# Optimization experiments

Hardware: AMD Instinct MI355X
Metric: run time of the kernel (lower is better)

Reference implementation:

```python
import jax, jax.numpy as jnp
import numpy as np

TEMPERATURE = 0.1
WINDOW = 7  # torch loop: k in range(1, min(8, seq_len - i)) -> offsets 1..7


def _normalize(x, axis=-1, eps=1e-12):
    # F.normalize: x / max(||x||, eps)
    n = jnp.linalg.norm(x, axis=axis, keepdims=True)
    return x / jnp.maximum(n, eps)


def setup_inputs() -> dict:
    key = jax.random.key(0)
    k1, k2 = jax.random.split(key, 2)
    states = jax.random.normal(k1, (4, 16, 1024, 256), dtype=jnp.float32)
    patterns = jax.random.normal(k2, (64, 256), dtype=jnp.float32)
    transfer_weights = jnp.zeros((16, 64, 64), dtype=jnp.float32)
    return {"states": states, "patterns": patterns, "transfer_weights": transfer_weights}


def _forward(states, patterns, transfer_weights):
    b, h, s, d = states.shape
    # --- detect_patterns: similarity to normalized pattern library + softmax ---
    sims = jnp.einsum('bhsd,pd->bhsp', states, _normalize(patterns))
    pattern_scores = jax.nn.softmax(sims / TEMPERATURE, axis=-1)  # [b,h,s,p]

    # --- compute_routing_scores: grad of states.sum() wrt states is ones ->
    #     grad_norm = ||ones||_2 over dim = sqrt(d) (constant), softmax over seq ---
    grad_norm = jnp.full((b, h, s), jnp.sqrt(jnp.float32(d)), dtype=states.dtype)
    routing_scores = jax.nn.softmax(grad_norm / TEMPERATURE, axis=-1)  # uniform [b,h,s]

    # --- optimize_routing: windowed min-plus shortest-path DP ---
    # torch keeps distances [b,h,s,s] but every slice along dim 2 is identical
    # (init and updates only index the last axis), so carry a [b,h,s] vector
    # and broadcast at the end. Pad by WINDOW so near-end updates land in pad.
    inf = jnp.float32(np.inf)
    dist0 = jnp.full((b, h, s + WINDOW), inf, dtype=states.dtype).at[..., 0].set(0.0)
    cost_pad = jnp.pad(-routing_scores, ((0, 0), (0, 0), (0, WINDOW)))

    def step(dist, i):
        cur = jax.lax.dynamic_slice_in_dim(dist, i, 1, axis=-1)          # [b,h,1]
        win = jax.lax.dynamic_slice_in_dim(dist, i + 1, WINDOW, axis=-1)  # [b,h,W]
        c = jax.lax.dynamic_slice_in_dim(cost_pad, i + 1, WINDOW, axis=-1)
        new = jnp.minimum(win, cur + c)
        dist = jax.lax.dynamic_update_slice_in_dim(dist, new, i + 1, axis=-1)
        return dist, None

    dist, _ = jax.lax.scan(step, dist0, jnp.arange(s - 1))
    d_final = dist[..., :s]                                  # [b,h,s]
    optimal_routes = jnp.broadcast_to(d_final[:, :, None, :], (b, h, s, s))

    return routing_scores, optimal_routes, transfer_weights, pattern_scores


def reference(states, patterns, transfer_weights):
    return _forward(states, patterns, transfer_weights)
```

## Files before the change

### kernel.cpp

```cpp
#include <hip/hip_runtime.h>
#include <math.h>

constexpr int B = 4, H = 16, S = 1024, D = 256, P = 64;
constexpr long long N_ROWS = (long long)B * H * S;
constexpr long long OFF_RT = 0;
constexpr long long SZ_RT  = N_ROWS;
constexpr long long OFF_OR = OFF_RT + SZ_RT;
constexpr long long SZ_OR  = N_ROWS * (long long)S;
constexpr long long OFF_TW = OFF_OR + SZ_OR;
constexpr long long SZ_TW  = 16LL * 64 * 64;
constexpr long long OFF_PS = OFF_TW + SZ_TW;

typedef _Float16 half8   __attribute__((ext_vector_type(8)));
typedef _Float16 half4v  __attribute__((ext_vector_type(4)));
typedef float    floatx4 __attribute__((ext_vector_type(4)));

constexpr int BSTRIDE = 264;

__global__ __launch_bounds__(64) void k_normalize(const float* __restrict__ pat,
                                                  _Float16* __restrict__ pnh,
                                                  _Float16* __restrict__ pnl) {
    int p    = blockIdx.x;
    int lane = threadIdx.x;
    const floatx4* src = (const floatx4*)(pat + (long long)p * D);
    floatx4 v = src[lane];
    float ss = v.x * v.x + v.y * v.y + v.z * v.z + v.w * v.w;
    #pragma unroll
    for (int m = 1; m < 64; m <<= 1) ss += __shfl_xor(ss, m, 64);
    float scale = 10.0f / fmaxf(sqrtf(ss), 1e-12f);
    float a[4] = { v.x * scale, v.y * scale, v.z * scale, v.w * scale };
    half4v hh, ll;
    #pragma unroll
    for (int j = 0; j < 4; ++j) {
        _Float16 h = (_Float16)a[j];
        hh[j] = h;
        ll[j] = (_Float16)(a[j] - (float)h);
    }
    *(half4v*)(pnh + (long long)p * D + lane * 4) = hh;
    *(half4v*)(pnl + (long long)p * D + lane * 4) = ll;
}

__global__ __launch_bounds__(256) void k_routes_small(
        floatx4* __restrict__ routes,
        const floatx4* __restrict__ tw,
        float* __restrict__ out) {
    long long blk = blockIdx.x;
    int t = threadIdx.x;
    if (blk < 65536) {
        long long i = blk * 256 + t;
        int j0 = (int)((i << 2) & (S - 1));
        float b0 = (float)j0 * (-0.0009765625f);
        floatx4 v;
        v.x = b0;
        v.y = b0 - 0.0009765625f;
        v.z = b0 - 0.001953125f;
        v.w = b0 - 0.0029296875f;
        routes[i] = v;
    } else {
        int i = (int)(blk - 65536) * 256 + t;
        constexpr int Q = (int)SZ_RT / 4;
        if (i < Q) {
            floatx4 v = { 0.0009765625f, 0.0009765625f,
                          0.0009765625f, 0.0009765625f };
            ((floatx4*)(out + OFF_RT))[i] = v;
        } else {
            ((floatx4*)(out + OFF_TW))[i - Q] = tw[i - Q];
        }
    }
}

__global__ __launch_bounds__(256) void k_gemm_mfma(
        const float* __restrict__ states,
        const _Float16* __restrict__ pnh,
        const _Float16* __restrict__ pnl,
        float* __restrict__ out_ps) {
    __shared__ _Float16 smem[2 * P * BSTRIDE];
    _Float16* smH = smem;
    _Float16* smL = smem + P * BSTRIDE;

    int tid  = threadIdx.x;
    {
        const half8* gh = (const half8*)pnh;
        const half8* gl = (const half8*)pnl;
        #pragma unroll
        for (int it = 0; it < 8; ++it) {
            int idx = it * 256 + tid;
            int row = idx >> 5;
            int c8  = idx & 31;
            *(half8*)&smH[row * BSTRIDE + c8 * 8] = gh[idx];
            *(half8*)&smL[row * BSTRIDE + c8 * 8] = gl[idx];
        }
    }
    __syncthreads();

    int wave = tid >> 6;
    int lane = tid & 63;
    int q    = lane >> 4;
    int m    = lane & 15;
    long long row0 = (long long)blockIdx.x * 64 + wave * 16;
    const float* __restrict__ arow = states + (row0 + m) * D + q * 8;

    floatx4 acc[4] = {floatx4{0,0,0,0}, floatx4{0,0,0,0},
                      floatx4{0,0,0,0}, floatx4{0,0,0,0}};

    float4 n0 = *(const float4*)(arow);
    float4 n1 = *(const float4*)(arow + 4);
    #pragma unroll
    for (int kk = 0; kk < 8; ++kk) {
        float4 a0 = n0, a1 = n1;
        if (kk < 7) {
            n0 = *(const float4*)(arow + (kk + 1) * 32);
            n1 = *(const float4*)(arow + (kk + 1) * 32 + 4);
        }
        float av[8] = { a0.x, a0.y, a0.z, a0.w, a1.x, a1.y, a1.z, a1.w };
        half8 ah, al;
        #pragma unroll
        for (int j = 0; j < 8; ++j) {
            _Float16 h = (_Float16)av[j];
            ah[j] = h;
            al[j] = (_Float16)(av[j] - (float)h);
        }
        #pragma unroll
        for (int t = 0; t < 4; ++t) {
            int boff = (t * 16 + m) * BSTRIDE + kk * 32 + q * 8;
            half8 bh = *(const half8*)&smH[boff];
            half8 bl = *(const half8*)&smL[boff];
            acc[t] = __builtin_amdgcn_mfma_f32_16x16x32_f16(ah, bh, acc[t], 0, 0, 0);
            acc[t] = __builtin_amdgcn_mfma_f32_16x16x32_f16(al, bh, acc[t], 0, 0, 0);
            acc[t] = __builtin_amdgcn_mfma_f32_16x16x32_f16(ah, bl, acc[t], 0, 0, 0);
        }
    }

    float e[4][4];
    #pragma unroll
    for (int r = 0; r < 4; ++r) {
        float mx = fmaxf(fmaxf(acc[0][r], acc[1][r]), fmaxf(acc[2][r], acc[3][r]));
        #pragma unroll
        for (int msk = 1; msk < 16; msk <<= 1) mx = fmaxf(mx, __shfl_xor(mx, msk, 64));
        float s = 0.0f;
        #pragma unroll
        for (int t = 0; t < 4; ++t) { e[t][r] = __expf(acc[t][r] - mx); s += e[t][r]; }
        #pragma unroll
        for (int msk = 1; msk < 16; msk <<= 1) s += __shfl_xor(s, msk, 64);
        float inv = 1.0f / s;
        long long row = row0 + q * 4 + r;
        #pragma unroll
        for (int t = 0; t < 4; ++t) {
            out_ps[row * P + t * 16 + m] = e[t][r] * inv;
        }
    }
}

extern "C" void kernel_launch(void* const* d_in, const int* in_sizes, int n_in,
                              void* d_out, int out_size, void* d_ws, size_t ws_size,
                              hipStream_t stream) {
    const float* states   = (const float*)d_in[0];
    const float* patterns = (const float*)d_in[1];
    const float* transfer = (const float*)d_in[2];
    float* out = (float*)d_out;
    _Float16* pnh = (_Float16*)d_ws;
    _Float16* pnl = pnh + P * D;

    k_normalize<<<dim3(P), dim3(64), 0, stream>>>(patterns, pnh, pnl);

    k_routes_small<<<dim3(65536 + 128), dim3(256), 0, stream>>>(
        (floatx4*)(out + OFF_OR), (const floatx4*)transfer, out);

    k_gemm_mfma<<<dim3(1024), dim3(256), 0, stream>>>(states, pnh, pnl, out + OFF_PS);
}
```

Baseline: 330.9 us.

## Fold pattern normalization into fill kernel and double rows per wave in GEMM

The separate pattern-normalize kernel is merged into the routes/fill kernel as 16 extra blocks, which removes one kernel launch. The GEMM kernel now has each wave process 32 rows instead of 16 with two accumulator sets, and the grid is halved to 512 blocks. This reuses each LDS B-fragment load across twice as many MFMAs and gives the loads more independent work to hide behind. The cost is higher register pressure and fewer blocks to spread across the CUs.

```diff
diff --git a/kernel.cpp b/kernel.cpp
--- a/kernel.cpp
+++ b/kernel.cpp
@@ -17,33 +17,13 @@
 
 constexpr int BSTRIDE = 264;
 
-__global__ __launch_bounds__(64) void k_normalize(const float* __restrict__ pat,
-                                                  _Float16* __restrict__ pnh,
-                                                  _Float16* __restrict__ pnl) {
-    int p    = blockIdx.x;
-    int lane = threadIdx.x;
-    const floatx4* src = (const floatx4*)(pat + (long long)p * D);
-    floatx4 v = src[lane];
-    float ss = v.x * v.x + v.y * v.y + v.z * v.z + v.w * v.w;
-    #pragma unroll
-    for (int m = 1; m < 64; m <<= 1) ss += __shfl_xor(ss, m, 64);
-    float scale = 10.0f / fmaxf(sqrtf(ss), 1e-12f);
-    float a[4] = { v.x * scale, v.y * scale, v.z * scale, v.w * scale };
-    half4v hh, ll;
-    #pragma unroll
-    for (int j = 0; j < 4; ++j) {
-        _Float16 h = (_Float16)a[j];
-        hh[j] = h;
-        ll[j] = (_Float16)(a[j] - (float)h);
-    }
-    *(half4v*)(pnh + (long long)p * D + lane * 4) = hh;
-    *(half4v*)(pnl + (long long)p * D + lane * 4) = ll;
-}
-
-__global__ __launch_bounds__(256) void k_routes_small(
+__global__ __launch_bounds__(256) void k_fill_prep(
         floatx4* __restrict__ routes,
         const floatx4* __restrict__ tw,
-        float* __restrict__ out) {
+        float* __restrict__ out,
+        const float* __restrict__ pat,
+        _Float16* __restrict__ pnh,
+        _Float16* __restrict__ pnl) {
     long long blk = blockIdx.x;
     int t = threadIdx.x;
     if (blk < 65536) {
@@ -56,7 +36,7 @@
         v.z = b0 - 0.001953125f;
         v.w = b0 - 0.0029296875f;
         routes[i] = v;
-    } else {
+    } else if (blk < 65536 + 128) {
         int i = (int)(blk - 65536) * 256 + t;
         constexpr int Q = (int)SZ_RT / 4;
         if (i < Q) {
@@ -66,6 +46,25 @@
         } else {
             ((floatx4*)(out + OFF_TW))[i - Q] = tw[i - Q];
         }
+    } else {
+        int p    = (int)(blk - 65536 - 128) * 4 + (t >> 6);
+        int lane = t & 63;
+        const floatx4* src = (const floatx4*)(pat + (long long)p * D);
+        floatx4 v = src[lane];
+        float ss = v.x * v.x + v.y * v.y + v.z * v.z + v.w * v.w;
+        #pragma unroll
+        for (int m = 1; m < 64; m <<= 1) ss += __shfl_xor(ss, m, 64);
+        float scale = 10.0f / fmaxf(sqrtf(ss), 1e-12f);
+        float a[4] = { v.x * scale, v.y * scale, v.z * scale, v.w * scale };
+        half4v hh, ll;
+        #pragma unroll
+        for (int j = 0; j < 4; ++j) {
+            _Float16 h = (_Float16)a[j];
+            hh[j] = h;
+            ll[j] = (_Float16)(a[j] - (float)h);
+        }
+        *(half4v*)(pnh + (long long)p * D + lane * 4) = hh;
+        *(half4v*)(pnl + (long long)p * D + lane * 4) = ll;
     }
 }
 
@@ -97,56 +96,76 @@
     int lane = tid & 63;
     int q    = lane >> 4;
     int m    = lane & 15;
-    long long row0 = (long long)blockIdx.x * 64 + wave * 16;
-    const float* __restrict__ arow = states + (row0 + m) * D + q * 8;
+    long long row0 = (long long)blockIdx.x * 128 + wave * 32;
+    const float* __restrict__ arow0 = states + (row0 + m) * D + q * 8;
+    const float* __restrict__ arow1 = arow0 + 16 * D;
 
-    floatx4 acc[4] = {floatx4{0,0,0,0}, floatx4{0,0,0,0},
-                      floatx4{0,0,0,0}, floatx4{0,0,0,0}};
+    floatx4 acc0[4] = {floatx4{0,0,0,0}, floatx4{0,0,0,0},
+                       floatx4{0,0,0,0}, floatx4{0,0,0,0}};
+    floatx4 acc1[4] = {floatx4{0,0,0,0}, floatx4{0,0,0,0},
+                       floatx4{0,0,0,0}, floatx4{0,0,0,0}};
 
-    float4 n0 = *(const float4*)(arow);
-    float4 n1 = *(const float4*)(arow + 4);
+    float4 n0 = *(const float4*)(arow0);
+    float4 n1 = *(const float4*)(arow0 + 4);
+    float4 n2 = *(const float4*)(arow1);
+    float4 n3 = *(const float4*)(arow1 + 4);
     #pragma unroll
     for (int kk = 0; kk < 8; ++kk) {
-        float4 a0 = n0, a1 = n1;
+        float av0[8] = { n0.x, n0.y, n0.z, n0.w, n1.x, n1.y, n1.z, n1.w };
+        float av1[8] = { n2.x, n2.y, n2.z, n2.w, n3.x, n3.y, n3.z, n3.w };
         if (kk < 7) {
-            n0 = *(const float4*)(arow + (kk + 1) * 32);
-            n1 = *(const float4*)(arow + (kk + 1) * 32 + 4);
+            n0 = *(const float4*)(arow0 + (kk + 1) * 32);
+            n1 = *(const float4*)(arow0 + (kk + 1) * 32 + 4);
+            n2 = *(const float4*)(arow1 + (kk + 1) * 32);
+            n3 = *(const float4*)(arow1 + (kk + 1) * 32 + 4);
         }
-        float av[8] = { a0.x, a0.y, a0.z, a0.w, a1.x, a1.y, a1.z, a1.w };
-        half8 ah, al;
+        half8 ah0, al0, ah1, al1;
         #pragma unroll
         for (int j = 0; j < 8; ++j) {
-            _Float16 h = (_Float16)av[j];
-            ah[j] = h;
-            al[j] = (_Float16)(av[j] - (float)h);
+            _Float16 h0 = (_Float16)av0[j];
+            ah0[j] = h0;
+            al0[j] = (_Float16)(av0[j] - (float)h0);
+            _Float16 h1 = (_Float16)av1[j];
+            ah1[j] = h1;
+            al1[j] = (_Float16)(av1[j] - (float)h1);
         }
         #pragma unroll
         for (int t = 0; t < 4; ++t) {
             int boff = (t * 16 + m) * BSTRIDE + kk * 32 + q * 8;
             half8 bh = *(const half8*)&smH[boff];
             half8 bl = *(const half8*)&smL[boff];
-            acc[t] = __builtin_amdgcn_mfma_f32_16x16x32_f16(ah, bh, acc[t], 0, 0, 0);
-            acc[t] = __builtin_amdgcn_mfma_f32_16x16x32_f16(al, bh, acc[t], 0, 0, 0);
-            acc[t] = __builtin_amdgcn_mfma_f32_16x16x32_f16(ah, bl, acc[t], 0, 0, 0);
+            acc0[t] = __builtin_amdgcn_mfma_f32_16x16x32_f16(ah0, bh, acc0[t], 0, 0, 0);
+            acc0[t] = __builtin_amdgcn_mfma_f32_16x16x32_f16(al0, bh, acc0[t], 0, 0, 0);
+            acc0[t] = __builtin_amdgcn_mfma_f32_16x16x32_f16(ah0, bl, acc0[t], 0, 0, 0);
+            acc1[t] = __builtin_amdgcn_mfma_f32_16x16x32_f16(ah1, bh, acc1[t], 0, 0, 0);
+            acc1[t] = __builtin_amdgcn_mfma_f32_16x16x32_f16(al1, bh, acc1[t], 0, 0, 0);
+            acc1[t] = __builtin_amdgcn_mfma_f32_16x16x32_f16(ah1, bl, acc1[t], 0, 0, 0);
         }
     }
 
-    float e[4][4];
     #pragma unroll
-    for (int r = 0; r < 4; ++r) {
-        float mx = fmaxf(fmaxf(acc[0][r], acc[1][r]), fmaxf(acc[2][r], acc[3][r]));
+    for (int set = 0; set < 2; ++set) {
+        floatx4* acc = set ? acc1 : acc0;
+        long long rbase = row0 + set * 16;
         #pragma unroll
-        for (int msk = 1; msk < 16; msk <<= 1) mx = fmaxf(mx, __shfl_xor(mx, msk, 64));
-        float s = 0.0f;
-        #pragma unroll
-        for (int t = 0; t < 4; ++t) { e[t][r] = __expf(acc[t][r] - mx); s += e[t][r]; }
-        #pragma unroll
-        for (int msk = 1; msk < 16; msk <<= 1) s += __shfl_xor(s, msk, 64);
-        float inv = 1.0f / s;
-        long long row = row0 + q * 4 + r;
-        #pragma unroll
-        for (int t = 0; t < 4; ++t) {
-            out_ps[row * P + t * 16 + m] = e[t][r] * inv;
+        for (int r = 0; r < 4; ++r) {
+            float mx = fmaxf(fmaxf(acc[0][r], acc[1][r]),
+                             fmaxf(acc[2][r], acc[3][r]));
+            #pragma unroll
+            for (int msk = 1; msk < 16; msk <<= 1)
+                mx = fmaxf(mx, __shfl_xor(mx, msk, 64));
+            float e[4];
+            float s = 0.0f;
+            #pragma unroll
+            for (int t = 0; t < 4; ++t) { e[t] = __expf(acc[t][r] - mx); s += e[t]; }
+            #pragma unroll
+            for (int msk = 1; msk < 16; msk <<= 1) s += __shfl_xor(s, msk, 64);
+            float inv = 1.0f / s;
+            long long row = rbase + q * 4 + r;
+            #pragma unroll
+            for (int t = 0; t < 4; ++t) {
+                out_ps[row * P + t * 16 + m] = e[t] * inv;
+            }
         }
     }
 }
@@ -161,10 +180,9 @@
     _Float16* pnh = (_Float16*)d_ws;
     _Float16* pnl = pnh + P * D;
 
-    k_normalize<<<dim3(P), dim3(64), 0, stream>>>(patterns, pnh, pnl);
+    k_fill_prep<<<dim3(65536 + 128 + 16), dim3(256), 0, stream>>>(
+        (floatx4*)(out + OFF_OR), (const floatx4*)transfer, out,
+        patterns, pnh, pnl);
 
-    k_routes_small<<<dim3(65536 + 128), dim3(256), 0, stream>>>(
-        (floatx4*)(out + OFF_OR), (const floatx4*)transfer, out);
-
-    k_gemm_mfma<<<dim3(1024), dim3(256), 0, stream>>>(states, pnh, pnl, out + OFF_PS);
+    k_gemm_mfma<<<dim3(512), dim3(256), 0, stream>>>(states, pnh, pnl, out + OFF_PS);
 }
```

Result: no change. 325.5 us (median of 2 runs) (-1.6%).
